# Kernel optimization log

Measured on AMD Instinct MI355X. Metric: run time of the kernel, lower is better.

The kernel has to match this reference:

```python
import jax, jax.numpy as jnp
import numpy as np

K = 5                                   # kernel_sz
SIGMA_SPATIAL = 2.0
SIGMA_INTENSITY = 0.1
NEG_SS_DIV = -1.0 / (2.0 * SIGMA_SPATIAL ** 2.0)   # value stored in self.kernel (same for all K*K taps)
SI_DIV = 1.0 / (2.0 * SIGMA_INTENSITY ** 2.0)      # self.sigma_intensity_div


def setup_inputs() -> dict:
    key = jax.random.key(0)
    k1, k2 = jax.random.split(key)
    t = jax.random.uniform(k1, (2, 3, 720, 1280), dtype=jnp.float32)      # guide image in [0,1]
    vector_curr = jax.random.normal(k2, (2, 2, 720, 1280), dtype=jnp.float32)  # flow vectors
    return {"t": t, "vector_curr": vector_curr}


def _joint_bilateral(t, v):
    # Fused sliding-window formulation: instead of materializing (N,H,W,K^2,C)
    # unfold patches, loop over the K*K static offsets (zero padding = F.unfold default)
    # and accumulate the weighted sum / normalizer. Same math as the original.
    N, C, H, W = t.shape
    Cv = v.shape[1]
    p = K // 2
    tp = jnp.pad(t, ((0, 0), (0, 0), (p, p), (p, p)))
    vp = jnp.pad(v, ((0, 0), (0, 0), (p, p), (p, p)))
    num = jnp.zeros_like(v)                      # (N,Cv,H,W)
    den = jnp.zeros((N, 1, H, W), t.dtype)
    for dy in range(K):
        for dx in range(K):
            ts = jax.lax.slice(tp, (0, 0, dy, dx), (N, C, dy + H, dx + W))
            vs = jax.lax.slice(vp, (0, 0, dy, dx), (N, Cv, dy + H, dx + W))
            # intensity_diff summed over guide channels -> (N,1,H,W)
            intensity_diff = jnp.sum((t - ts) ** 2, axis=1, keepdims=True)
            # coeff = clamp(1 - |kernel - diff * sigma_intensity_div|, 0, 1)
            coeff = jnp.clip(1.0 - jnp.abs(NEG_SS_DIV - intensity_diff * SI_DIV), 0.0, 1.0)
            num = num + vs * coeff
            den = den + coeff
    return (num / den).astype(jnp.float16)       # original returns fp16 NCHW


def reference(t, vector_curr):
    return _joint_bilateral(t, vector_curr)
```

## Files before the change

### kernel.cpp

```cpp
#include <hip/hip_runtime.h>
#include <hip/hip_fp16.h>


constexpr int H_ = 720;
constexpr int W_ = 1280;
constexpr int HW = H_ * W_;
constexpr float COEF0 = 0.875f;
constexpr float SIDIV = 50.0f;

constexpr int TC = 132;
constexpr int TR = 12;
constexpr int NK = 34;
constexpr int NCHUNK = 5 * TR * NK;
constexpr int NXCD = 8;
constexpr int CPX = 1800 / NXCD;

#define LOADW(LR)                                                              \
    float w0[8], w1[8], w2[8], u0[8], u1[8];                                   \
    _Pragma("unroll") for (int s_ = 0; s_ < 2; ++s_) {                         \
        *(float4*)(w0 + 4 * s_) = *(const float4*)&lds[0][LR][lc + 4 * s_];    \
        *(float4*)(w1 + 4 * s_) = *(const float4*)&lds[1][LR][lc + 4 * s_];    \
        *(float4*)(w2 + 4 * s_) = *(const float4*)&lds[2][LR][lc + 4 * s_];    \
        *(float4*)(u0 + 4 * s_) = *(const float4*)&lds[3][LR][lc + 4 * s_];    \
        *(float4*)(u1 + 4 * s_) = *(const float4*)&lds[4][LR][lc + 4 * s_];    \
    }

#define COMPW()                                                                \
    _Pragma("unroll") for (int dx_ = 0; dx_ < 5; ++dx_)                        \
        _Pragma("unroll") for (int j_ = 0; j_ < 4; ++j_) {                     \
            const int k_ = dx_ + j_;                                           \
            const float d0_ = c0f[j_] - w0[k_];                                \
            const float d1_ = c1f[j_] - w1[k_];                                \
            const float d2_ = c2f[j_] - w2[k_];                                \
            float diff_ = d0_ * d0_;                                           \
            diff_ = fmaf(d1_, d1_, diff_);                                     \
            diff_ = fmaf(d2_, d2_, diff_);                                     \
            const float c_ = fmaxf(fmaf(diff_, -SIDIV, COEF0), 0.f);           \
            num0[j_] = fmaf(u0[k_], c_, num0[j_]);                             \
            num1[j_] = fmaf(u1[k_], c_, num1[j_]);                             \
            den[j_] += c_;                                                     \
        }

__global__ __launch_bounds__(256)
void jbf_mlp(const float* __restrict__ t, const float* __restrict__ v,
             float* __restrict__ out) {
    __shared__ float lds[5][TR][TC];

    const int wgid = (blockIdx.x & (NXCD - 1)) * CPX + (blockIdx.x >> 3);
    const int n   = wgid / 900;
    const int rem = wgid % 900;
    const int by  = rem / 10;
    const int bx  = rem % 10;
    const int gx0 = bx * 128;
    const int gy0 = by * 8;

    const float* tn = t + (size_t)n * 3 * HW;
    const float* vn = v + (size_t)n * 2 * HW;
    float*       on = out + (size_t)n * 2 * HW;

    const int tid = threadIdx.x;

    float4 vals[8];
#pragma unroll
    for (int it = 0; it < 8; ++it) {
        const int i = tid + it * 256;
        const int k  = i % NK;
        const int rr = (i / NK) % TR;
        const int ch = i / (NK * TR);
        const int gy = gy0 - 2 + rr;
        const int gx = gx0 - 4 + 4 * k;
        vals[it] = make_float4(0.f, 0.f, 0.f, 0.f);
        const bool live = (it < 7 || i < NCHUNK) &&
                          ((unsigned)gy < (unsigned)H_) &&
                          ((unsigned)gx < (unsigned)(W_ - 3));
        if (live) {
            const float* src = (ch < 3) ? (tn + (size_t)ch * HW)
                                        : (vn + (size_t)(ch - 3) * HW);
            vals[it] = *(const float4*)(src + gy * W_ + gx);
        }
    }

#pragma unroll
    for (int it = 0; it < 8; ++it) {
        const int i = tid + it * 256;
        if (it < 7 || i < NCHUNK) {
            const int k  = i % NK;
            const int rr = (i / NK) % TR;
            const int ch = i / (NK * TR);
            float* row = &lds[ch][rr][0];
            const float4 val = vals[it];
            if (k > 0)      *(float2*)&row[4 * k - 2] = make_float2(val.x, val.y);
            if (k < NK - 1) *(float2*)&row[4 * k]     = make_float2(val.z, val.w);
        }
    }
    __syncthreads();

    const int tx = tid & 31;
    const int ty = tid >> 5;
    const int lc = 4 * tx;

    float c0f[4], c1f[4], c2f[4];
    float num0[4] = {0.f, 0.f, 0.f, 0.f};
    float num1[4] = {0.f, 0.f, 0.f, 0.f};
    float den[4]  = {0.f, 0.f, 0.f, 0.f};

    {
        const int lr = ty + 2;
        LOADW(lr)
#pragma unroll
        for (int j = 0; j < 4; ++j) {
            c0f[j] = w0[j + 2];
            c1f[j] = w1[j + 2];
            c2f[j] = w2[j + 2];
        }
        COMPW()
    }
#pragma unroll 1
    for (int i = 0; i < 4; ++i) {
        const int r = i + (i >> 1);
        const int lr = ty + r;
        LOADW(lr)
        COMPW()
    }

    float4 o0, o1;
    float* o0a = (float*)&o0;
    float* o1a = (float*)&o1;
#pragma unroll
    for (int j = 0; j < 4; ++j) {
        const float rcp = 1.f / den[j];
        o0a[j] = __half2float(__float2half(num0[j] * rcp));
        o1a[j] = __half2float(__float2half(num1[j] * rcp));
    }
    const int ctr = (gy0 + ty) * W_ + gx0 + 4 * tx;
    *(float4*)(on + ctr) = o0;
    *(float4*)(on + HW + ctr) = o1;
}

extern "C" void kernel_launch(void* const* d_in, const int* in_sizes, int n_in,
                              void* d_out, int out_size, void* d_ws, size_t ws_size,
                              hipStream_t stream) {
    const float* t = (const float*)d_in[0];
    const float* v = (const float*)d_in[1];
    float* out = (float*)d_out;

    jbf_mlp<<<1800, 256, 0, stream>>>(t, v, out);
}
```

Before: 26.46 us.

## Process two tiles per block with register-prefetch of the second tile

The grid shrinks from 1800 to 1280 blocks, and the first 520 blocks handle two tiles each. While computing on tile A out of LDS, the block prefetches tile B's global loads into registers, then writes them to LDS and computes tile B. This is meant to hide global-load latency behind compute and cut the tail wave of the 1800-block launch. The cost is load imbalance, since some blocks do twice the work, plus the register pressure of keeping the prefetched values live during compute.

```diff
diff --git a/kernel.cpp b/kernel.cpp
--- a/kernel.cpp
+++ b/kernel.cpp
@@ -13,7 +13,60 @@
 constexpr int NK = 34;
 constexpr int NCHUNK = 5 * TR * NK;
 constexpr int NXCD = 8;
-constexpr int CPX = 1800 / NXCD;
+constexpr int NTILES = 1800;
+constexpr int GRID = 1280;
+constexpr int CPX = NTILES / NXCD;
+
+__device__ __forceinline__ void decode_tile(int vid, int& n, int& gx0, int& gy0) {
+    const int wgid = (vid & (NXCD - 1)) * CPX + (vid >> 3);
+    n = wgid / 900;
+    const int rem = wgid % 900;
+    gy0 = (rem / 10) * 8;
+    gx0 = (rem % 10) * 128;
+}
+
+__device__ __forceinline__ void load_tile(const float* __restrict__ t,
+                                          const float* __restrict__ v,
+                                          int n, int gx0, int gy0, int tid,
+                                          float4 (&vals)[8]) {
+    const float* tn = t + (size_t)n * 3 * HW;
+    const float* vn = v + (size_t)n * 2 * HW;
+#pragma unroll
+    for (int it = 0; it < 8; ++it) {
+        const int i = tid + it * 256;
+        const int k  = i % NK;
+        const int rr = (i / NK) % TR;
+        const int ch = i / (NK * TR);
+        const int gy = gy0 - 2 + rr;
+        const int gx = gx0 - 4 + 4 * k;
+        vals[it] = make_float4(0.f, 0.f, 0.f, 0.f);
+        const bool live = (it < 7 || i < NCHUNK) &&
+                          ((unsigned)gy < (unsigned)H_) &&
+                          ((unsigned)gx < (unsigned)(W_ - 3));
+        if (live) {
+            const float* src = (ch < 3) ? (tn + (size_t)ch * HW)
+                                        : (vn + (size_t)(ch - 3) * HW);
+            vals[it] = *(const float4*)(src + gy * W_ + gx);
+        }
+    }
+}
+
+__device__ __forceinline__ void write_tile(float (*lds)[TR][TC], int tid,
+                                           const float4 (&vals)[8]) {
+#pragma unroll
+    for (int it = 0; it < 8; ++it) {
+        const int i = tid + it * 256;
+        if (it < 7 || i < NCHUNK) {
+            const int k  = i % NK;
+            const int rr = (i / NK) % TR;
+            const int ch = i / (NK * TR);
+            float* row = &lds[ch][rr][0];
+            const float4 val = vals[it];
+            if (k > 0)      *(float2*)&row[4 * k - 2] = make_float2(val.x, val.y);
+            if (k < NK - 1) *(float2*)&row[4 * k]     = make_float2(val.z, val.w);
+        }
+    }
+}
 
 #define LOADW(LR)                                                              \
     float w0[8], w1[8], w2[8], u0[8], u1[8];                                   \
@@ -41,60 +94,10 @@
             den[j_] += c_;                                                     \
         }
 
-__global__ __launch_bounds__(256)
-void jbf_mlp(const float* __restrict__ t, const float* __restrict__ v,
-             float* __restrict__ out) {
-    __shared__ float lds[5][TR][TC];
-
-    const int wgid = (blockIdx.x & (NXCD - 1)) * CPX + (blockIdx.x >> 3);
-    const int n   = wgid / 900;
-    const int rem = wgid % 900;
-    const int by  = rem / 10;
-    const int bx  = rem % 10;
-    const int gx0 = bx * 128;
-    const int gy0 = by * 8;
-
-    const float* tn = t + (size_t)n * 3 * HW;
-    const float* vn = v + (size_t)n * 2 * HW;
-    float*       on = out + (size_t)n * 2 * HW;
-
-    const int tid = threadIdx.x;
-
-    float4 vals[8];
-#pragma unroll
-    for (int it = 0; it < 8; ++it) {
-        const int i = tid + it * 256;
-        const int k  = i % NK;
-        const int rr = (i / NK) % TR;
-        const int ch = i / (NK * TR);
-        const int gy = gy0 - 2 + rr;
-        const int gx = gx0 - 4 + 4 * k;
-        vals[it] = make_float4(0.f, 0.f, 0.f, 0.f);
-        const bool live = (it < 7 || i < NCHUNK) &&
-                          ((unsigned)gy < (unsigned)H_) &&
-                          ((unsigned)gx < (unsigned)(W_ - 3));
-        if (live) {
-            const float* src = (ch < 3) ? (tn + (size_t)ch * HW)
-                                        : (vn + (size_t)(ch - 3) * HW);
-            vals[it] = *(const float4*)(src + gy * W_ + gx);
-        }
-    }
-
-#pragma unroll
-    for (int it = 0; it < 8; ++it) {
-        const int i = tid + it * 256;
-        if (it < 7 || i < NCHUNK) {
-            const int k  = i % NK;
-            const int rr = (i / NK) % TR;
-            const int ch = i / (NK * TR);
-            float* row = &lds[ch][rr][0];
-            const float4 val = vals[it];
-            if (k > 0)      *(float2*)&row[4 * k - 2] = make_float2(val.x, val.y);
-            if (k < NK - 1) *(float2*)&row[4 * k]     = make_float2(val.z, val.w);
-        }
-    }
-    __syncthreads();
-
+__device__ __forceinline__ void compute_store(const float (*lds)[TR][TC],
+                                              float* __restrict__ out,
+                                              int n, int gx0, int gy0, int tid) {
+    float* on = out + (size_t)n * 2 * HW;
     const int tx = tid & 31;
     const int ty = tid >> 5;
     const int lc = 4 * tx;
@@ -137,6 +140,36 @@
     *(float4*)(on + HW + ctr) = o1;
 }
 
+__global__ __launch_bounds__(256)
+void jbf_pp(const float* __restrict__ t, const float* __restrict__ v,
+            float* __restrict__ out) {
+    __shared__ float lds[5][TR][TC];
+
+    const int tid = threadIdx.x;
+    const bool two = ((int)blockIdx.x < NTILES - GRID);
+
+    int nA, gxA, gyA;
+    decode_tile(blockIdx.x, nA, gxA, gyA);
+
+    float4 vals[8];
+    load_tile(t, v, nA, gxA, gyA, tid, vals);
+    write_tile(lds, tid, vals);
+    __syncthreads();
+
+    if (two) {
+        int nB, gxB, gyB;
+        decode_tile((int)blockIdx.x + GRID, nB, gxB, gyB);
+        load_tile(t, v, nB, gxB, gyB, tid, vals);
+        compute_store(lds, out, nA, gxA, gyA, tid);
+        __syncthreads();
+        write_tile(lds, tid, vals);
+        __syncthreads();
+        compute_store(lds, out, nB, gxB, gyB, tid);
+    } else {
+        compute_store(lds, out, nA, gxA, gyA, tid);
+    }
+}
+
 extern "C" void kernel_launch(void* const* d_in, const int* in_sizes, int n_in,
                               void* d_out, int out_size, void* d_ws, size_t ws_size,
                               hipStream_t stream) {
@@ -144,5 +177,5 @@
     const float* v = (const float*)d_in[1];
     float* out = (float*)d_out;
 
-    jbf_mlp<<<1800, 256, 0, stream>>>(t, v, out);
+    jbf_pp<<<GRID, 256, 0, stream>>>(t, v, out);
 }
```

Measured after the change: 27.09 us. 1.02x slower.
